# Performance work log

Measured on AMD Instinct MI355X. Metric: run time of the kernel, lower is better.

The kernel has to match this reference:

```python
import jax, jax.numpy as jnp
import numpy as np
import math

B, T, C, H = 2, 2048, 1024, 16
HD = C // H  # head dim = 64

def setup_inputs() -> dict:
    key = jax.random.key(0)
    ks = jax.random.split(key, 12)
    s = 0.02
    return {
        "x": jax.random.normal(ks[0], (B, T, C), dtype=jnp.float32),
        "ln1_g": jnp.ones((C,), jnp.float32),
        "ln1_b": jnp.zeros((C,), jnp.float32),
        "W_attn": jax.random.normal(ks[1], (C, 3 * C), jnp.float32) * s,
        "b_attn": jnp.zeros((3 * C,), jnp.float32),
        "W_ap": jax.random.normal(ks[2], (C, C), jnp.float32) * s,
        "b_ap": jnp.zeros((C,), jnp.float32),
        "ln2_g": jnp.ones((C,), jnp.float32),
        "ln2_b": jnp.zeros((C,), jnp.float32),
        "W_fc": jax.random.normal(ks[3], (C, 4 * C), jnp.float32) * s,
        "b_fc": jnp.zeros((4 * C,), jnp.float32),
        "W_mp": jax.random.normal(ks[4], (4 * C, C), jnp.float32) * s,
        "b_mp": jnp.zeros((C,), jnp.float32),
    }

def layernorm(x, g, b, eps=1e-5):
    mu = jnp.mean(x, axis=-1, keepdims=True)
    var = jnp.mean(jnp.square(x - mu), axis=-1, keepdims=True)
    return (x - mu) * jax.lax.rsqrt(var + eps) * g + b

def gelu_tanh(x):
    # GELU(approximate='tanh')
    c = math.sqrt(2.0 / math.pi)
    return 0.5 * x * (1.0 + jnp.tanh(c * (x + 0.044715 * x * x * x)))

def attention(x, W_attn, b_attn, W_ap, b_ap):
    b, t, c = x.shape
    qkv = x @ W_attn + b_attn                      # [B,T,3C]
    q, k, v = jnp.split(qkv, 3, axis=-1)
    q = q.reshape(b, t, H, HD).transpose(0, 2, 1, 3)  # [B,H,T,hd]
    k = k.reshape(b, t, H, HD).transpose(0, 2, 1, 3)
    v = v.reshape(b, t, H, HD).transpose(0, 2, 1, 3)
    attn = jnp.einsum('bhqd,bhkd->bhqk', q, k) * (1.0 / math.sqrt(HD))
    mask = jnp.tril(jnp.ones((t, t), dtype=bool))
    attn = jnp.where(mask, attn, jnp.float32(-jnp.inf))
    attn = jax.nn.softmax(attn, axis=-1)
    y = jnp.einsum('bhqk,bhkd->bhqd', attn, v)
    y = y.transpose(0, 2, 1, 3).reshape(b, t, c)
    return y @ W_ap + b_ap

def reference(x, ln1_g, ln1_b, W_attn, b_attn, W_ap, b_ap,
              ln2_g, ln2_b, W_fc, b_fc, W_mp, b_mp):
    x = x + attention(layernorm(x, ln1_g, ln1_b), W_attn, b_attn, W_ap, b_ap)
    h = layernorm(x, ln2_g, ln2_b)
    h = gelu_tanh(h @ W_fc + b_fc) @ W_mp + b_mp
    return x + h
```

## Files before the change

kernel.cpp:

```cpp
#include <hip/hip_runtime.h>
#include <stdint.h>

#define TT_ 2048
#define CC_ 1024

typedef unsigned short u16;
typedef __bf16 bf16x8 __attribute__((ext_vector_type(8)));
typedef __bf16 bf16x4 __attribute__((ext_vector_type(4)));
typedef float f32x4 __attribute__((ext_vector_type(4)));
typedef unsigned short u16x8 __attribute__((ext_vector_type(8)));

__device__ __forceinline__ u16 f2bf(float f) {
  unsigned u = __float_as_uint(f);
  u += 0x7fff + ((u >> 16) & 1);
  return (u16)(u >> 16);
}
__device__ __forceinline__ float bf2f(u16 v) {
  return __uint_as_float(((unsigned)v) << 16);
}

__device__ __forceinline__ float gelu_f(float t) {
  float u = 1.5957691216057308f * (t + 0.044715f * t * t * t);
  return t / (1.f + __expf(-u));
}

__device__ __forceinline__ void async_cp16(const u16* g, u16* l) {
  __builtin_amdgcn_global_load_lds(
      (const __attribute__((address_space(1))) void*)(uintptr_t)g,
      (__attribute__((address_space(3))) void*)(uint32_t)(uintptr_t)l,
      16, 0, 0);
}

__device__ __forceinline__ void blockbar() {
  asm volatile("" ::: "memory");
  __builtin_amdgcn_s_barrier();
  asm volatile("" ::: "memory");
}

__global__ __launch_bounds__(256) void kconv_t(const float* __restrict__ W,
                                               u16* __restrict__ WT, int K, int N) {
  __shared__ float t[32][33];
  int n0 = blockIdx.x * 32, k0 = blockIdx.y * 32;
  int tx = threadIdx.x & 31, ty = threadIdx.x >> 5;
#pragma unroll
  for (int r = 0; r < 4; ++r)
    t[ty + 8 * r][tx] = W[(size_t)(k0 + ty + 8 * r) * N + n0 + tx];
  __syncthreads();
#pragma unroll
  for (int r = 0; r < 4; ++r)
    WT[(size_t)(n0 + ty + 8 * r) * K + k0 + tx] = f2bf(t[tx][ty + 8 * r]);
}

__global__ __launch_bounds__(256) void kln(const float* __restrict__ x,
                                           const float* __restrict__ g,
                                           const float* __restrict__ b,
                                           u16* __restrict__ out) {
  int row = blockIdx.x, tid = threadIdx.x;
  const float4* xr = (const float4*)(x + (size_t)row * CC_);
  float4 v = xr[tid];
  float s = v.x + v.y + v.z + v.w;
  float s2 = v.x * v.x + v.y * v.y + v.z * v.z + v.w * v.w;
#pragma unroll
  for (int off = 32; off; off >>= 1) { s += __shfl_down(s, off); s2 += __shfl_down(s2, off); }
  __shared__ float rs[4], rq[4];
  int w = tid >> 6;
  if ((tid & 63) == 0) { rs[w] = s; rq[w] = s2; }
  __syncthreads();
  s = rs[0] + rs[1] + rs[2] + rs[3];
  s2 = rq[0] + rq[1] + rq[2] + rq[3];
  float mean = s * (1.f / CC_);
  float var = s2 * (1.f / CC_) - mean * mean;
  float rstd = rsqrtf(var + 1e-5f);
  float4 gv = ((const float4*)g)[tid];
  float4 bv = ((const float4*)b)[tid];
  u16* orow = out + (size_t)row * CC_ + tid * 4;
  orow[0] = f2bf((v.x - mean) * rstd * gv.x + bv.x);
  orow[1] = f2bf((v.y - mean) * rstd * gv.y + bv.y);
  orow[2] = f2bf((v.z - mean) * rstd * gv.z + bv.z);
  orow[3] = f2bf((v.w - mean) * rstd * gv.w + bv.w);
}

template <int EPI, int NSPLIT>
__global__ __launch_bounds__(256) void kgemm(const u16* __restrict__ A,
                                             const u16* __restrict__ BTm,
                                             const float* __restrict__ bias,
                                             const float* __restrict__ resid,
                                             void* __restrict__ out,
                                             u16* __restrict__ part,
                                             int M, int N, int Ktot) {
  __shared__ __align__(16) u16 As[2][128 * 32];
  __shared__ __align__(16) u16 Bs[2][128 * 32];
  const int tid = threadIdx.x, lane = tid & 63, w = tid >> 6;
  const int llo = lane & 15, lhi = lane >> 4;
  const int row0 = blockIdx.y * 128, col0 = blockIdx.x * 128;
  const int wr = w >> 1, wc = w & 1;
  const int crow = lane >> 2;
  const int ck = (lane & 3) * 8;
  const int Kc = Ktot / NSPLIT;
  const int klo = (NSPLIT > 1) ? blockIdx.z * Kc : 0;

  f32x4 acc[4][4] = {};

  auto stage = [&](int bufi, int kof) {
#pragma unroll
    for (int c = w; c < 8; c += 4) {
      int r = c * 16 + crow;
      async_cp16(A + (size_t)(row0 + r) * Ktot + klo + kof + ck, &As[bufi][c * 512]);
      async_cp16(BTm + (size_t)(col0 + r) * Ktot + klo + kof + ck, &Bs[bufi][c * 512]);
    }
  };

  const int nt = Kc / 32;
  stage(0, 0);
  asm volatile("s_waitcnt vmcnt(0)" ::: "memory");
  blockbar();
  int cur = 0;

  for (int t = 0; t < nt; ++t) {
    if (t + 1 < nt) stage(cur ^ 1, (t + 1) * 32);
    bf16x8 af[4], bfr[4];
#pragma unroll
    for (int m = 0; m < 4; ++m)
      af[m] = *(const bf16x8*)&As[cur][(wr * 64 + m * 16 + llo) * 32 + lhi * 8];
#pragma unroll
    for (int n = 0; n < 4; ++n)
      bfr[n] = *(const bf16x8*)&Bs[cur][(wc * 64 + n * 16 + llo) * 32 + lhi * 8];
#pragma unroll
    for (int m = 0; m < 4; ++m)
#pragma unroll
      for (int n = 0; n < 4; ++n)
        acc[m][n] = __builtin_amdgcn_mfma_f32_16x16x32_bf16(af[m], bfr[n], acc[m][n], 0, 0, 0);
    if (t + 1 < nt) {
      asm volatile("s_waitcnt vmcnt(0)" ::: "memory");
      blockbar();
    }
    cur ^= 1;
  }

  const int c_row = row0 + wr * 64 + lhi * 4;
  const int c_col = col0 + wc * 64 + llo;
  const bool fin = (NSPLIT == 1) || (blockIdx.z == 0);
  u16* pb = part + (NSPLIT > 1 ? ((size_t)(blockIdx.z > 0 ? blockIdx.z - 1 : 0)) * M * N : 0);
#pragma unroll
  for (int n = 0; n < 4; ++n) {
    int col = c_col + n * 16;
    float bb = bias[col];
#pragma unroll
    for (int m = 0; m < 4; ++m) {
      f32x4 a = acc[m][n];
#pragma unroll
      for (int i = 0; i < 4; ++i) {
        size_t idx = (size_t)(c_row + m * 16 + i) * N + col;
        if (!fin) {
          pb[idx] = f2bf(a[i]);
        } else {
          float val = a[i] + bb;
          if constexpr (EPI == 1) {
            ((float*)out)[idx] = val + resid[idx];
          } else if constexpr (EPI == 2) {
            ((u16*)out)[idx] = f2bf(gelu_f(val));
          } else {
            ((u16*)out)[idx] = f2bf(val);
          }
        }
      }
    }
  }
}

template <int NP>
__global__ __launch_bounds__(256) void kaddN(float* __restrict__ out,
                                             const u16* __restrict__ p, size_t MN) {
  size_t i0 = ((size_t)blockIdx.x * 256 + threadIdx.x) * 8;
  float4 o0 = *(float4*)(out + i0);
  float4 o1 = *(float4*)(out + i0 + 4);
#pragma unroll
  for (int s = 0; s < NP; ++s) {
    u16x8 v = *(const u16x8*)(p + (size_t)s * MN + i0);
    o0.x += bf2f(v[0]); o0.y += bf2f(v[1]); o0.z += bf2f(v[2]); o0.w += bf2f(v[3]);
    o1.x += bf2f(v[4]); o1.y += bf2f(v[5]); o1.z += bf2f(v[6]); o1.w += bf2f(v[7]);
  }
  *(float4*)(out + i0) = o0;
  *(float4*)(out + i0 + 4) = o1;
}

__global__ __launch_bounds__(256) void kvtrans(const u16* __restrict__ qkv,
                                               u16* __restrict__ VT) {
  int tt = blockIdx.x;
  int bh = blockIdx.y;
  int b = bh >> 4, h = bh & 15;
  __shared__ u16 t[64][72];
  int r = threadIdx.x >> 3, c0 = (threadIdx.x & 7) * 8;
  const u16* src = qkv + (size_t)(b * TT_ + tt * 64) * 3072 + 2048 + h * 64;
#pragma unroll
  for (int it = 0; it < 2; ++it) {
    int rr = r + it * 32;
    *(u16x8*)&t[rr][c0] = *(const u16x8*)(src + (size_t)rr * 3072 + c0);
  }
  __syncthreads();
  u16* dst = VT + ((size_t)bh * 64) * TT_ + tt * 64;
#pragma unroll
  for (int it = 0; it < 2; ++it) {
    int d = r + it * 32;
    u16x8 v;
#pragma unroll
    for (int e = 0; e < 8; ++e) v[e] = t[c0 + e][d];
    *(u16x8*)(dst + (size_t)d * TT_ + c0) = v;
  }
}

__global__ __launch_bounds__(256, 4) void kattn(const u16* __restrict__ qkv,
                                                const u16* __restrict__ VT,
                                                u16* __restrict__ y) {
  const int h = blockIdx.x, b = blockIdx.y, z = blockIdx.z;
  const int tid = threadIdx.x, lane = tid & 63, w = tid >> 6;
  const int llo = lane & 15, lhi = lane >> 4;

  __shared__ __align__(16) u16 Qs[64 * 64];
  __shared__ __align__(16) u16 Ks[2][64 * 64];
  __shared__ __align__(16) u16 Vs[2][64 * 64];
  __shared__ __align__(16) u16 Ps[64 * 72];

  const size_t tok0 = (size_t)b * TT_;
  const u16* qb = qkv + tok0 * 3072 + h * 64;
  const u16* kb = qb + 1024;

  const u16 *kg[2], *vg[2];
#pragma unroll
  for (int it = 0; it < 2; ++it) {
    int p_ = w * 16 + it * 8 + (lane >> 3);
    int krow = ((p_ & 15) << 2) | (p_ >> 4);
    int scol = ((lane & 7) * 8) ^ ((p_ & 7) << 3);
    kg[it] = kb + (size_t)krow * 3072 + scol;
    vg[it] = VT + ((size_t)(b * 16 + h) * 64 + p_) * TT_ + scol;
  }

  auto stageKV = [&](int bufi, int j) {
    async_cp16(kg[0] + (size_t)j * (64 * 3072), &Ks[bufi][(w * 16 + 0) * 64]);
    async_cp16(kg[1] + (size_t)j * (64 * 3072), &Ks[bufi][(w * 16 + 8) * 64]);
    async_cp16(vg[0] + (size_t)j * 64, &Vs[bufi][(w * 16 + 0) * 64]);
    async_cp16(vg[1] + (size_t)j * 64, &Vs[bufi][(w * 16 + 8) * 64]);
  };

  const float alpha = 0.18033688011112042f;
  const int r8 = tid >> 3, ce = (tid & 7) * 8;

#pragma unroll 1
  for (int ph = 0; ph < 2; ++ph) {
    const int qt = ph ? (31 - z) : z;
    const int q0 = qt * 64;

#pragma unroll
    for (int it = 0; it < 2; ++it) {
      int tk = it * 32 + r8;
      u16x8 v = *(const u16x8*)(qb + (size_t)(q0 + tk) * 3072 + ce);
#pragma unroll
      for (int e = 0; e < 8; ++e) v[e] = f2bf(bf2f(v[e]) * alpha);
      *(u16x8*)&Qs[tk * 64 + (ce ^ ((tk & 7) << 3))] = v;
    }
    asm volatile("s_waitcnt lgkmcnt(0)" ::: "memory");
    stageKV(0, 0);
    blockbar();

    bf16x8 aq[2];
#pragma unroll
    for (int kk = 0; kk < 2; ++kk)
      aq[kk] = *(const bf16x8*)&Qs[(w * 16 + llo) * 64 +
                                   ((kk * 32 + lhi * 8) ^ ((llo & 7) << 3))];

    float m_i[4], l_i[4];
    f32x4 o[4] = {};
#pragma unroll
    for (int i = 0; i < 4; ++i) { m_i[i] = -1e30f; l_i[i] = 0.f; }

    int buf = 0;
    for (int j = 0; j <= qt; ++j) {
      if (j < qt) {
        stageKV(buf ^ 1, j + 1);
        asm volatile("s_waitcnt vmcnt(4)" ::: "memory");
      } else {
        asm volatile("s_waitcnt vmcnt(0)" ::: "memory");
      }
      blockbar();

      f32x4 s[4] = {};
      __builtin_amdgcn_s_setprio(1);
#pragma unroll
      for (int nb = 0; nb < 4; ++nb)
#pragma unroll
        for (int kk = 0; kk < 2; ++kk) {
          bf16x8 bk = *(const bf16x8*)&Ks[buf][(nb * 16 + llo) * 64 +
                                              ((kk * 32 + lhi * 8) ^ ((llo & 7) << 3))];
          s[nb] = __builtin_amdgcn_mfma_f32_16x16x32_bf16(aq[kk], bk, s[nb], 0, 0, 0);
        }
      __builtin_amdgcn_s_setprio(0);

      float sc[4][4];
      if (j == qt) {
#pragma unroll
        for (int nb = 0; nb < 4; ++nb)
#pragma unroll
          for (int i = 0; i < 4; ++i) {
            float v = s[nb][i];
            if (llo * 4 + nb > w * 16 + lhi * 4 + i) v = -1e30f;
            sc[nb][i] = v;
          }
      } else {
#pragma unroll
        for (int nb = 0; nb < 4; ++nb)
#pragma unroll
          for (int i = 0; i < 4; ++i) sc[nb][i] = s[nb][i];
      }

      float rm[4];
#pragma unroll
      for (int i = 0; i < 4; ++i) {
        float r = fmaxf(fmaxf(sc[0][i], sc[1][i]), fmaxf(sc[2][i], sc[3][i]));
#pragma unroll
        for (int off = 1; off < 16; off <<= 1) r = fmaxf(r, __shfl_xor(r, off));
        rm[i] = r;
      }

      bool need = (rm[0] > m_i[0] + 8.f) | (rm[1] > m_i[1] + 8.f) |
                  (rm[2] > m_i[2] + 8.f) | (rm[3] > m_i[3] + 8.f);
      if (__any(need)) {
#pragma unroll
        for (int i = 0; i < 4; ++i) {
          float mn = fmaxf(m_i[i], rm[i]);
          float corr = exp2f(m_i[i] - mn);
          l_i[i] *= corr;
#pragma unroll
          for (int db = 0; db < 4; ++db) o[db][i] *= corr;
          m_i[i] = mn;
        }
      }

#pragma unroll
      for (int i = 0; i < 4; ++i) {
        float p0 = exp2f(sc[0][i] - m_i[i]);
        float p1 = exp2f(sc[1][i] - m_i[i]);
        float p2 = exp2f(sc[2][i] - m_i[i]);
        float p3 = exp2f(sc[3][i] - m_i[i]);
        l_i[i] += (p0 + p1) + (p2 + p3);
        bf16x4 pk = {(__bf16)p0, (__bf16)p1, (__bf16)p2, (__bf16)p3};
        *(bf16x4*)&Ps[(w * 16 + lhi * 4 + i) * 72 + llo * 4] = pk;
      }

      bf16x8 pa[2];
#pragma unroll
      for (int kk = 0; kk < 2; ++kk)
        pa[kk] = *(const bf16x8*)&Ps[(w * 16 + llo) * 72 + kk * 32 + lhi * 8];
      __builtin_amdgcn_s_setprio(1);
#pragma unroll
      for (int db = 0; db < 4; ++db)
#pragma unroll
        for (int kk = 0; kk < 2; ++kk) {
          bf16x8 bv = *(const bf16x8*)&Vs[buf][(db * 16 + llo) * 64 +
                                              ((kk * 32 + lhi * 8) ^ ((llo & 7) << 3))];
          o[db] = __builtin_amdgcn_mfma_f32_16x16x32_bf16(pa[kk], bv, o[db], 0, 0, 0);
        }
      __builtin_amdgcn_s_setprio(0);
      blockbar();
      buf ^= 1;
    }

#pragma unroll
    for (int i = 0; i < 4; ++i) {
      float t = l_i[i];
#pragma unroll
      for (int off = 1; off < 16; off <<= 1) t += __shfl_xor(t, off);
      float inv = 1.f / t;
      size_t row = tok0 + q0 + w * 16 + lhi * 4 + i;
#pragma unroll
      for (int db = 0; db < 4; ++db)
        y[row * CC_ + h * 64 + db * 16 + llo] = f2bf(o[db][i] * inv);
    }
  }
}

extern "C" void kernel_launch(void* const* d_in, const int* in_sizes, int n_in,
                              void* d_out, int out_size, void* d_ws, size_t ws_size,
                              hipStream_t stream) {
  (void)in_sizes; (void)n_in; (void)out_size; (void)ws_size;
  const float* x      = (const float*)d_in[0];
  const float* ln1g   = (const float*)d_in[1];
  const float* ln1b   = (const float*)d_in[2];
  const float* W_attn = (const float*)d_in[3];
  const float* b_attn = (const float*)d_in[4];
  const float* W_ap   = (const float*)d_in[5];
  const float* b_ap   = (const float*)d_in[6];
  const float* ln2g   = (const float*)d_in[7];
  const float* ln2b   = (const float*)d_in[8];
  const float* W_fc   = (const float*)d_in[9];
  const float* b_fc   = (const float*)d_in[10];
  const float* W_mp   = (const float*)d_in[11];
  const float* b_mp   = (const float*)d_in[12];

  char* p = (char*)d_ws;
  u16* WTmp   = (u16*)p; p += (size_t)4096 * 1024 * 2;
  u16* WTattn = (u16*)p; p += (size_t)3072 * 1024 * 2;
  u16* WTap   = (u16*)p; p += (size_t)1024 * 1024 * 2;
  u16* WTfc   = (u16*)p; p += (size_t)4096 * 1024 * 2;
  u16* xn     = (u16*)p; p += (size_t)4096 * 1024 * 2;
  u16* qkvb   = (u16*)p; p += (size_t)4096 * 3072 * 2;
  u16* yb     = (u16*)p; p += (size_t)4096 * 1024 * 2;
  float* x1   = (float*)p; p += (size_t)4096 * 1024 * 4;
  u16* h2     = (u16*)p; p += (size_t)4096 * 1024 * 2;
  u16* fcb    = qkvb;
  u16* VT     = (u16*)x1;
  u16* appart = xn;
  u16* mpp    = WTattn;

  kconv_t<<<dim3(96, 32), 256, 0, stream>>>(W_attn, WTattn, 1024, 3072);
  kconv_t<<<dim3(32, 32), 256, 0, stream>>>(W_ap, WTap, 1024, 1024);
  kconv_t<<<dim3(128, 32), 256, 0, stream>>>(W_fc, WTfc, 1024, 4096);
  kconv_t<<<dim3(32, 128), 256, 0, stream>>>(W_mp, WTmp, 4096, 1024);

  kln<<<4096, 256, 0, stream>>>(x, ln1g, ln1b, xn);
  kgemm<0, 1><<<dim3(24, 32), 256, 0, stream>>>(xn, WTattn, b_attn, nullptr, qkvb, nullptr, 4096, 3072, 1024);
  kvtrans<<<dim3(32, 32), 256, 0, stream>>>(qkvb, VT);
  kattn<<<dim3(16, 2, 16), 256, 0, stream>>>(qkvb, VT, yb);
  kgemm<1, 2><<<dim3(8, 32, 2), 256, 0, stream>>>(yb, WTap, b_ap, x, x1, appart, 4096, 1024, 1024);
  kaddN<1><<<2048, 256, 0, stream>>>(x1, appart, (size_t)4096 * 1024);
  kln<<<4096, 256, 0, stream>>>(x1, ln2g, ln2b, h2);
  kgemm<2, 1><<<dim3(32, 32), 256, 0, stream>>>(h2, WTfc, b_fc, nullptr, fcb, nullptr, 4096, 4096, 1024);
  kgemm<1, 4><<<dim3(8, 32, 4), 256, 0, stream>>>(fcb, WTmp, b_mp, x1, (float*)d_out, mpp, 4096, 1024, 4096);
  kaddN<3><<<2048, 256, 0, stream>>>((float*)d_out, mpp, (size_t)4096 * 1024);
}
```

Baseline: 299.6 us.

## Remap GEMM blocks per XCD for L2 locality and reduce MLP-proj split-K

The GEMM kernel now takes a 1D grid and remaps block IDs so that blocks landing on the same XCD (bid & 7) cover a contiguous rectangular chunk of output tiles. Each XCD's L2 then reuses the A and B panels. The MLP projection GEMM also drops from split-K 4 to split-K 2, which halves the partial-sum traffic and simplifies the final reduction, at the cost of fewer blocks (512) and less parallelism. The mapping assumes grid sizes divide evenly into 8 XCD chunks.

```diff
diff --git a/kernel.cpp b/kernel.cpp
--- a/kernel.cpp
+++ b/kernel.cpp
@@ -87,17 +87,27 @@
                                              const float* __restrict__ resid,
                                              void* __restrict__ out,
                                              u16* __restrict__ part,
-                                             int M, int N, int Ktot) {
+                                             int M, int N, int Ktot,
+                                             int chunks_x, int ychunks, int cx) {
   __shared__ __align__(16) u16 As[2][128 * 32];
   __shared__ __align__(16) u16 Bs[2][128 * 32];
   const int tid = threadIdx.x, lane = tid & 63, w = tid >> 6;
   const int llo = lane & 15, lhi = lane >> 4;
-  const int row0 = blockIdx.y * 128, col0 = blockIdx.x * 128;
+
+  const int bid = blockIdx.x;
+  const int xcd = bid & 7, s = bid >> 3;
+  const int chx = xcd % chunks_x, chyz = xcd / chunks_x;
+  const int z = chyz / ychunks, chy = chyz % ychunks;
+  const int bx = chx * cx + s % cx;
+  const int cy = (gridDim.x >> 3) / cx;
+  const int by = chy * cy + s / cx;
+
+  const int row0 = by * 128, col0 = bx * 128;
   const int wr = w >> 1, wc = w & 1;
   const int crow = lane >> 2;
   const int ck = (lane & 3) * 8;
   const int Kc = Ktot / NSPLIT;
-  const int klo = (NSPLIT > 1) ? blockIdx.z * Kc : 0;
+  const int klo = (NSPLIT > 1) ? z * Kc : 0;
 
   f32x4 acc[4][4] = {};
 
@@ -139,8 +149,8 @@
 
   const int c_row = row0 + wr * 64 + lhi * 4;
   const int c_col = col0 + wc * 64 + llo;
-  const bool fin = (NSPLIT == 1) || (blockIdx.z == 0);
-  u16* pb = part + (NSPLIT > 1 ? ((size_t)(blockIdx.z > 0 ? blockIdx.z - 1 : 0)) * M * N : 0);
+  const bool fin = (NSPLIT == 1) || (z == 0);
+  u16* pb = part + (NSPLIT > 1 ? ((size_t)(z > 0 ? z - 1 : 0)) * M * N : 0);
 #pragma unroll
   for (int n = 0; n < 4; ++n) {
     int col = c_col + n * 16;
@@ -417,13 +427,17 @@
   kconv_t<<<dim3(32, 128), 256, 0, stream>>>(W_mp, WTmp, 4096, 1024);
 
   kln<<<4096, 256, 0, stream>>>(x, ln1g, ln1b, xn);
-  kgemm<0, 1><<<dim3(24, 32), 256, 0, stream>>>(xn, WTattn, b_attn, nullptr, qkvb, nullptr, 4096, 3072, 1024);
+  kgemm<0, 1><<<768, 256, 0, stream>>>(xn, WTattn, b_attn, nullptr, qkvb, nullptr,
+                                       4096, 3072, 1024, 2, 4, 12);
   kvtrans<<<dim3(32, 32), 256, 0, stream>>>(qkvb, VT);
   kattn<<<dim3(16, 2, 16), 256, 0, stream>>>(qkvb, VT, yb);
-  kgemm<1, 2><<<dim3(8, 32, 2), 256, 0, stream>>>(yb, WTap, b_ap, x, x1, appart, 4096, 1024, 1024);
+  kgemm<1, 2><<<512, 256, 0, stream>>>(yb, WTap, b_ap, x, x1, appart,
+                                       4096, 1024, 1024, 1, 4, 8);
   kaddN<1><<<2048, 256, 0, stream>>>(x1, appart, (size_t)4096 * 1024);
   kln<<<4096, 256, 0, stream>>>(x1, ln2g, ln2b, h2);
-  kgemm<2, 1><<<dim3(32, 32), 256, 0, stream>>>(h2, WTfc, b_fc, nullptr, fcb, nullptr, 4096, 4096, 1024);
-  kgemm<1, 4><<<dim3(8, 32, 4), 256, 0, stream>>>(fcb, WTmp, b_mp, x1, (float*)d_out, mpp, 4096, 1024, 4096);
-  kaddN<3><<<2048, 256, 0, stream>>>((float*)d_out, mpp, (size_t)4096 * 1024);
-}
+  kgemm<2, 1><<<1024, 256, 0, stream>>>(h2, WTfc, b_fc, nullptr, fcb, nullptr,
+                                        4096, 4096, 1024, 2, 4, 16);
+  kgemm<1, 2><<<512, 256, 0, stream>>>(fcb, WTmp, b_mp, x1, (float*)d_out, mpp,
+                                       4096, 1024, 4096, 1, 4, 8);
+  kaddN<1><<<2048, 256, 0, stream>>>((float*)d_out, mpp, (size_t)4096 * 1024);
+}
```

New measurement: 282.3 us. 1.06x faster.
